# Optimization experiments

Hardware: AMD Instinct MI355X
Metric: run time of the kernel (lower is better)

The kernel has to match this reference:

```python
import jax, jax.numpy as jnp
import numpy as np

L = 32      # num_layer
N_ORD = 64  # order_of_a_LTImodel
U = 64      # u_size
Y = 64      # y_size
T = 8192    # sequence length
SCALE = 0.05  # keep block-bidiagonal A spectrally stable over 8192 steps


def setup_inputs() -> dict:
    key = jax.random.key(0)
    k_u, k_a, k_b0, k_bl, k_c = jax.random.split(key, 5)
    inp = {
        "input": jax.random.normal(k_u, (T, U), dtype=jnp.float32),
        # per-layer A_i weights (diagonal blocks)
        "A_stack": jax.random.normal(k_a, (L, N_ORD, N_ORD), dtype=jnp.float32) * SCALE,
        # layer-0 B (maps u -> state)
        "B0": jax.random.normal(k_b0, (N_ORD, U), dtype=jnp.float32) * SCALE,
        # layer i>=1 B weights (sub-diagonal coupling blocks)
        "B_lower": jax.random.normal(k_bl, (L - 1, N_ORD, N_ORD), dtype=jnp.float32) * SCALE,
        # per-layer C_i weights, concatenated along columns in forward
        "C_stack": jax.random.normal(k_c, (L, Y, N_ORD), dtype=jnp.float32),
        # D is frozen zeros (feedthrough=False)
        "D_w": jnp.zeros((Y, U), dtype=jnp.float32),
    }
    return inp


def _assemble(A_stack, B0, B_lower, C_stack):
    l, n, _ = A_stack.shape
    S = l * n
    A = jnp.zeros((S, S), A_stack.dtype)
    for i in range(l):  # fixed small structural loop
        A = A.at[i * n:(i + 1) * n, i * n:(i + 1) * n].set(A_stack[i])
    for i in range(1, l):
        A = A.at[i * n:(i + 1) * n, (i - 1) * n:i * n].set(B_lower[i - 1])
    B = jnp.concatenate([B0, jnp.zeros((S - n, B0.shape[1]), B0.dtype)], axis=0)
    # torch.cat([C_i], dim=1): [Y, L*n]
    C = jnp.transpose(C_stack, (1, 0, 2)).reshape(C_stack.shape[1], S)
    return A, B, C


def reference(input, A_stack, B0, B_lower, C_stack, D_w):
    A, B, C = _assemble(A_stack, B0, B_lower, C_stack)
    S = A.shape[0]
    x0 = jnp.zeros((S,), input.dtype)

    def step(x, u):
        y = C @ x + D_w @ u      # output BEFORE state update (y_t uses x_t)
        x_next = A @ x + B @ u
        return x_next, y

    _, ys = jax.lax.scan(step, x0, input)
    return ys  # [T, Y]
```

## Files before the change

kernel.cpp:

```cpp
#include <hip/hip_runtime.h>


#define LYR 32
#define NO  64
#define TSEQ 8192
#define PAD 32
#define PR2 (TSEQ+PAD)
#define PB2 ((size_t)PR2*NO)
#define KQ  2048

typedef _Float16 h16;
typedef _Float16 h16x8 __attribute__((ext_vector_type(8)));
typedef float    f32x4 __attribute__((ext_vector_type(4)));

#define MFMA16(a,b,c) __builtin_amdgcn_mfma_f32_16x16x32_f16((a),(b),(c),0,0,0)

__global__ __launch_bounds__(256) void prep_build(
    const float* __restrict__ u, const float* __restrict__ B0,
    const float* __restrict__ Bl, const float* __restrict__ Cst,
    const float* __restrict__ Ast,
    h16* __restrict__ xq, h16* __restrict__ ccast,
    h16* __restrict__ SN, h16* __restrict__ ST,
    h16* __restrict__ ktq, float* __restrict__ Dacc)
{
    __shared__ float sm[3*64*68];
    const int tid = threadIdx.x;

    if (blockIdx.x < 32) {
        const int layer = blockIdx.x;
        float* la = sm;
        float* kc = sm + 64*68;
        float* kn = sm + 2*64*68;
        const float* k0 = (layer == 0) ? B0 : (Bl + (size_t)(layer-1)*4096);
        const float* Aw = Ast + (size_t)layer*4096;
        for (int e = tid; e < 4096; e += 256) {
            int rr = e >> 6, cc = e & 63;
            kc[rr*68 + cc] = k0[e];
            la[rr*68 + cc] = Aw[e];
        }
        __syncthreads();
        const int r0 = (tid >> 4) << 2;
        const int c0 = (tid & 15) << 2;
        for (int j = 0; j < 16; j++) {
            if (j > 0) {
                __syncthreads();
                float acc[4][4] = {};
                for (int k = 0; k < 64; k++) {
                    float a0 = la[(r0+0)*68 + k];
                    float a1 = la[(r0+1)*68 + k];
                    float a2 = la[(r0+2)*68 + k];
                    float a3 = la[(r0+3)*68 + k];
                    f32x4 bv = *(const f32x4*)&kc[k*68 + c0];
                    #pragma unroll
                    for (int jj = 0; jj < 4; jj++) {
                        acc[0][jj] += a0*bv[jj]; acc[1][jj] += a1*bv[jj];
                        acc[2][jj] += a2*bv[jj]; acc[3][jj] += a3*bv[jj];
                    }
                }
                #pragma unroll
                for (int i2 = 0; i2 < 4; i2++) {
                    f32x4 o; o[0]=acc[i2][0]; o[1]=acc[i2][1]; o[2]=acc[i2][2]; o[3]=acc[i2][3];
                    *(f32x4*)&kn[(r0+i2)*68 + c0] = o;
                }
                __syncthreads();
                float* tmp = kc; kc = kn; kn = tmp;
            }
            size_t base = (size_t)(layer*16 + j)*4096;
            for (int e8 = tid; e8 < 512; e8 += 256) {
                int n = e8 >> 3, m0 = (e8 & 7) << 3;
                h16 o[8];
                #pragma unroll
                for (int t = 0; t < 8; t++) o[t] = (h16)kc[n*68 + m0 + t];
                *(int4*)&SN[base + (size_t)n*64 + m0] = *(int4*)&o[0];
                h16 o2[8];
                #pragma unroll
                for (int t = 0; t < 8; t++) o2[t] = (h16)kc[(m0+t)*68 + n];
                *(int4*)&ST[base + (size_t)n*64 + m0] = *(int4*)&o2[0];
            }
        }
        return;
    }

    const int s1 = 256;
    const int s2 = 65536;
    const int s3 = 1792;
    const int s4 = 16384;
    const int s5 = 131072;
    const int s6 = 262144;
    const int total = s1+s2+s3+s4+s5+s6;
    const int4 z4 = make_int4(0,0,0,0);
    for (int e0 = (blockIdx.x - 32)*256 + tid; e0 < total; e0 += 512*256) {
        int e = e0;
        if (e < s1) { *(int4*)&xq[e*8] = z4; continue; }
        e -= s1;
        if (e < s2) {
            int el = e*8;
            f32x4 f0 = *(const f32x4*)&u[el];
            f32x4 f1 = *(const f32x4*)&u[el+4];
            h16 ov[8];
            #pragma unroll
            for (int j = 0; j < 4; j++) { ov[j] = (h16)f0[j]; ov[4+j] = (h16)f1[j]; }
            *(int4*)&xq[PAD*NO + el] = *(int4*)&ov[0];
            continue;
        }
        e -= s2;
        if (e < s3) {
            int b = e >> 8, off = (e & 255)*8;
            *(int4*)&xq[(size_t)(b+1)*PB2 + off] = z4;
            continue;
        }
        e -= s3;
        if (e < s4) {
            int el = e*8;
            f32x4 f0 = *(const f32x4*)&Cst[el];
            f32x4 f1 = *(const f32x4*)&Cst[el+4];
            h16 ov[8];
            #pragma unroll
            for (int j = 0; j < 4; j++) { ov[j] = (h16)f0[j]; ov[4+j] = (h16)f1[j]; }
            *(int4*)&ccast[el] = *(int4*)&ov[0];
            continue;
        }
        e -= s4;
        if (e < s5) { *(int4*)&ktq[e*8] = z4; continue; }
        e -= s5;
        *(int4*)&Dacc[e*4] = z4;
    }
}

__device__ __forceinline__ void comp_mm(const h16* __restrict__ X,
                                        const h16* __restrict__ Y,
                                        int wv, int r, int q, f32x4 acc[4])
{
    h16x8 a0 = *(const h16x8*)(X + (wv*16 + r)*64 + q*8);
    h16x8 a1 = *(const h16x8*)(X + (wv*16 + r)*64 + 32 + q*8);
    #pragma unroll
    for (int c = 0; c < 4; c++) {
        h16x8 b0 = *(const h16x8*)(Y + (c*16 + r)*64 + q*8);
        h16x8 b1 = *(const h16x8*)(Y + (c*16 + r)*64 + 32 + q*8);
        acc[c] = MFMA16(a0, b0, acc[c]);
        acc[c] = MFMA16(a1, b1, acc[c]);
    }
}

__global__ __launch_bounds__(256) void compose2(
    const h16* __restrict__ SN, const h16* __restrict__ ST,
    const h16* __restrict__ cc, h16* __restrict__ P2T,
    float* __restrict__ Dacc)
{
    const int tid = threadIdx.x, wv = tid>>6, lane = tid&63, r = lane&15, q = lane>>4;
    f32x4 acc[4] = {};
    int bid = blockIdx.x;
    if (bid < 248) {
        int g = bid / 31, m2 = bid % 31;
        int j0 = m2 > 15 ? m2 - 15 : 0;
        int j1 = m2 < 15 ? m2 : 15;
        const h16* X = SN + ((size_t)(4*g+1)*16 + j0)*4096;
        const h16* Y = ST + ((size_t)(4*g)*16 + (m2 - j0))*4096;
        for (int it = 0; it <= j1 - j0; ++it) {
            comp_mm(X, Y, wv, r, q, acc);
            X += 4096; Y -= 4096;
        }
        h16* o = P2T + ((size_t)g*31 + m2)*4096;
        #pragma unroll
        for (int c = 0; c < 4; c++)
            #pragma unroll
            for (int g4 = 0; g4 < 4; g4++)
                o[(c*16+r)*64 + wv*16 + q*4 + g4] = (h16)acc[c][g4];
    } else {
        int idx = bid - 248, g = idx >> 4, j = idx & 15;
        comp_mm(cc + (size_t)(4*g)*4096, ST + ((size_t)(4*g)*16 + j)*4096, wv, r, q, acc);
        float* Dd = Dacc + ((size_t)g*32 + j)*4096;
        #pragma unroll
        for (int c = 0; c < 4; c++)
            #pragma unroll
            for (int g4 = 0; g4 < 4; g4++)
                atomicAdd(&Dd[(wv*16 + q*4 + g4)*64 + c*16 + r], acc[c][g4]);
    }
}

__global__ __launch_bounds__(256) void compose3(
    const h16* __restrict__ SN, const h16* __restrict__ cc,
    const h16* __restrict__ P2T, h16* __restrict__ P3T,
    float* __restrict__ Dacc)
{
    const int tid = threadIdx.x, wv = tid>>6, lane = tid&63, r = lane&15, q = lane>>4;
    f32x4 acc[4] = {};
    int bid = blockIdx.x;
    if (bid < 240) {
        int g = bid / 30, m3 = bid % 30;
        int j1 = m3 < 15 ? m3 : 15;
        const h16* X = SN + ((size_t)(4*g+2)*16)*4096;
        const h16* Y = P2T + ((size_t)g*31 + m3)*4096;
        for (int it = 0; it <= j1; ++it) {
            comp_mm(X, Y, wv, r, q, acc);
            X += 4096; Y -= 4096;
        }
        h16* o = P3T + ((size_t)g*30 + m3)*4096;
        #pragma unroll
        for (int c = 0; c < 4; c++)
            #pragma unroll
            for (int g4 = 0; g4 < 4; g4++)
                o[(c*16+r)*64 + wv*16 + q*4 + g4] = (h16)acc[c][g4];
    } else {
        int idx = bid - 240, g = idx / 31, m2 = idx % 31;
        comp_mm(cc + (size_t)(4*g+1)*4096, P2T + ((size_t)g*31 + m2)*4096, wv, r, q, acc);
        float* Dd = Dacc + ((size_t)g*32 + m2 + 1)*4096;
        #pragma unroll
        for (int c = 0; c < 4; c++)
            #pragma unroll
            for (int g4 = 0; g4 < 4; g4++)
                atomicAdd(&Dd[(wv*16 + q*4 + g4)*64 + c*16 + r], acc[c][g4]);
    }
}

__global__ __launch_bounds__(256) void compose4(
    const h16* __restrict__ SN, const h16* __restrict__ cc,
    const h16* __restrict__ P3T, h16* __restrict__ ktq,
    float* __restrict__ Dacc)
{
    __shared__ h16 ldsT[64*72];
    const int tid = threadIdx.x, wv = tid>>6, lane = tid&63, r = lane&15, q = lane>>4;
    f32x4 acc[4] = {};
    int bid = blockIdx.x;
    if (bid < 232) {
        int g = bid / 29, m4 = bid % 29;
        int j1 = m4 < 15 ? m4 : 15;
        const h16* X = SN + ((size_t)(4*g+3)*16)*4096;
        const h16* Y = P3T + ((size_t)g*30 + m4)*4096;
        for (int it = 0; it <= j1; ++it) {
            comp_mm(X, Y, wv, r, q, acc);
            X += 4096; Y -= 4096;
        }
        h16* kq = ktq + (size_t)g*131072 + (size_t)(28 - m4)*64;
        #pragma unroll
        for (int c = 0; c < 4; c++)
            #pragma unroll
            for (int g4 = 0; g4 < 4; g4++) {
                h16 v = (h16)acc[c][g4];
                kq[(size_t)(wv*16 + q*4 + g4)*KQ + c*16 + r] = v;
                ldsT[(c*16+r)*72 + wv*16 + q*4 + g4] = v;
            }
        __syncthreads();
        f32x4 acc2[4] = {};
        const h16* Xc = cc + (size_t)(4*g+3)*4096;
        h16x8 a0 = *(const h16x8*)(Xc + (wv*16 + r)*64 + q*8);
        h16x8 a1 = *(const h16x8*)(Xc + (wv*16 + r)*64 + 32 + q*8);
        #pragma unroll
        for (int c = 0; c < 4; c++) {
            h16x8 b0 = *(const h16x8*)(&ldsT[(c*16+r)*72 + q*8]);
            h16x8 b1 = *(const h16x8*)(&ldsT[(c*16+r)*72 + 32 + q*8]);
            acc2[c] = MFMA16(a0, b0, acc2[c]);
            acc2[c] = MFMA16(a1, b1, acc2[c]);
        }
        float* Dd = Dacc + ((size_t)g*32 + m4 + 3)*4096;
        #pragma unroll
        for (int c = 0; c < 4; c++)
            #pragma unroll
            for (int g4 = 0; g4 < 4; g4++)
                atomicAdd(&Dd[(wv*16 + q*4 + g4)*64 + c*16 + r], acc2[c][g4]);
    } else {
        int idx = bid - 232, g = idx / 30, m3 = idx % 30;
        comp_mm(cc + (size_t)(4*g+2)*4096, P3T + ((size_t)g*30 + m3)*4096, wv, r, q, acc);
        float* Dd = Dacc + ((size_t)g*32 + m3 + 2)*4096;
        #pragma unroll
        for (int c = 0; c < 4; c++)
            #pragma unroll
            for (int g4 = 0; g4 < 4; g4++)
                atomicAdd(&Dd[(wv*16 + q*4 + g4)*64 + c*16 + r], acc[c][g4]);
    }
}

__global__ __launch_bounds__(256) void castD(const float* __restrict__ Dacc,
                                             h16* __restrict__ ktd)
{
    const int total4 = 8*32*4096/4;
    for (int idx4 = blockIdx.x*256 + threadIdx.x; idx4 < total4; idx4 += 256*256) {
        int idx = idx4 << 2;
        int gdo = idx >> 12;
        int g = gdo >> 5, dd = gdo & 31;
        int rem = idx & 4095;
        int y = rem >> 6, m = rem & 63;
        f32x4 f = *(const f32x4*)&Dacc[idx];
        h16 o4[4];
        #pragma unroll
        for (int t = 0; t < 4; t++) o4[t] = (h16)f[t];
        *(int2*)&ktd[(size_t)g*131072 + (size_t)y*KQ + (31 - dd)*64 + m] = *(int2*)&o4[0];
    }
}

template<int WRST>
__global__ __launch_bounds__(512) void stage(
    const h16* __restrict__ pin, h16* __restrict__ pout,
    const h16* __restrict__ ktqg, const h16* __restrict__ ktdg,
    float* __restrict__ out, int first)
{
    __shared__ __align__(16) h16   win[64*72];
    __shared__ __align__(16) float red[4*32*68];
    const int tid = threadIdx.x;
    const size_t t0 = (size_t)blockIdx.x * 32;

    {
        int rr = tid >> 3, cc = tid & 7;
        *(int4*)&win[rr*72 + cc*8] = *(const int4*)&pin[(t0 + rr)*64 + cc*8];
    }
    __syncthreads();

    const int wv = tid >> 6, lane = tid & 63, r = lane & 15, q = lane >> 4;
    const int half = wv >> 2, kq = wv & 3;
    const bool active = WRST || (half == 1);
    f32x4 acc[2][4] = {};
    if (active) {
        const h16* kb = half ? ktdg : ktqg;
        const h16* abase = &win[(r + kq*8)*72 + q*8];
        const h16* bbase = kb + (size_t)r*KQ + kq*512 + q*8;
#define LDA(s, ls) (*(const h16x8*)(abase + ((s)*16 + ((ls)>>1))*72 + ((ls)&1)*32))
#define LDB(c, ls) (*(const h16x8*)(bbase + (size_t)(c)*(16*KQ) + (ls)*32))
        h16x8 a[2][2], b[2][4];
        #pragma unroll
        for (int sl = 0; sl < 2; sl++) {
            #pragma unroll
            for (int s = 0; s < 2; s++) a[sl][s] = LDA(s, sl);
            #pragma unroll
            for (int c = 0; c < 4; c++) b[sl][c] = LDB(c, sl);
        }
        #pragma unroll
        for (int ls = 0; ls < 16; ls++) {
            h16x8 ca[2], cb[4];
            #pragma unroll
            for (int s = 0; s < 2; s++) ca[s] = a[ls&1][s];
            #pragma unroll
            for (int c = 0; c < 4; c++) cb[c] = b[ls&1][c];
            if (ls < 14) {
                #pragma unroll
                for (int s = 0; s < 2; s++) a[ls&1][s] = LDA(s, ls+2);
                #pragma unroll
                for (int c = 0; c < 4; c++) b[ls&1][c] = LDB(c, ls+2);
            }
            #pragma unroll
            for (int s = 0; s < 2; s++)
                #pragma unroll
                for (int c = 0; c < 4; c++)
                    acc[s][c] = MFMA16(ca[s], cb[c], acc[s][c]);
        }
#undef LDA
#undef LDB
    }

    const int rh = half * (2*32*68);
    __syncthreads();
    if (active && kq >= 2) {
        float* myred = red + rh + (kq-2)*(32*68);
        #pragma unroll
        for (int s2 = 0; s2 < 2; s2++)
            #pragma unroll
            for (int c = 0; c < 4; c++)
                #pragma unroll
                for (int g4 = 0; g4 < 4; g4++)
                    myred[(s2*16 + q*4 + g4)*68 + c*16 + r] = acc[s2][c][g4];
    }
    __syncthreads();
    if (active && kq < 2) {
        float* myred = red + rh + kq*(32*68);
        #pragma unroll
        for (int s2 = 0; s2 < 2; s2++)
            #pragma unroll
            for (int c = 0; c < 4; c++)
                #pragma unroll
                for (int g4 = 0; g4 < 4; g4++)
                    myred[(s2*16 + q*4 + g4)*68 + c*16 + r] += acc[s2][c][g4];
    }
    __syncthreads();
    if (WRST && tid < 256) {
        int orow = tid >> 3, cb2 = (tid & 7) << 3;
        f32x4 u0 = *(const f32x4*)&red[orow*68 + cb2];
        f32x4 u1 = *(const f32x4*)&red[orow*68 + cb2 + 4];
        f32x4 v0 = *(const f32x4*)&red[32*68 + orow*68 + cb2];
        f32x4 v1 = *(const f32x4*)&red[32*68 + orow*68 + cb2 + 4];
        u0 += v0; u1 += v1;
        h16 ov[8];
        #pragma unroll
        for (int j = 0; j < 4; j++) { ov[j] = (h16)u0[j]; ov[4+j] = (h16)u1[j]; }
        *(int4*)&pout[(PAD + t0 + orow)*64 + cb2] = *(int4*)&ov[0];
    }
    if (tid >= 256) {
        int t2 = tid - 256;
        int orow = t2 >> 3, cb2 = (t2 & 7) << 3;
        const float* base = red + 2*32*68;
        f32x4 u0 = *(const f32x4*)&base[orow*68 + cb2];
        f32x4 u1 = *(const f32x4*)&base[orow*68 + cb2 + 4];
        f32x4 v0 = *(const f32x4*)&base[32*68 + orow*68 + cb2];
        f32x4 v1 = *(const f32x4*)&base[32*68 + orow*68 + cb2 + 4];
        u0 += v0; u1 += v1;
        float* op = out + (t0 + orow)*64 + cb2;
        if (first) {
            *(f32x4*)op = u0; *(f32x4*)(op+4) = u1;
        } else {
            f32x4 o0 = *(f32x4*)op, o1 = *(f32x4*)(op+4);
            o0 += u0; o1 += u1;
            *(f32x4*)op = o0; *(f32x4*)(op+4) = o1;
        }
    }
}

extern "C" void kernel_launch(void* const* d_in, const int* in_sizes, int n_in,
                              void* d_out, int out_size, void* d_ws, size_t ws_size,
                              hipStream_t stream)
{
    const float* u   = (const float*)d_in[0];
    const float* Ast = (const float*)d_in[1];
    const float* B0  = (const float*)d_in[2];
    const float* Bl  = (const float*)d_in[3];
    const float* Cst = (const float*)d_in[4];
    float* out = (float*)d_out;
    (void)in_sizes; (void)n_in; (void)out_size; (void)ws_size;

    char* ws = (char*)d_ws;
    h16*   xq    = (h16*)ws;
    h16*   ccast = (h16*)(ws + 8421376);
    h16*   SN    = (h16*)(ws + 8683520);
    h16*   ST    = (h16*)(ws + 12877824);
    h16*   P2T   = (h16*)(ws + 17072128);
    h16*   P3T   = (h16*)(ws + 19103744);
    h16*   ktq   = (h16*)(ws + 21069824);
    h16*   ktd   = (h16*)(ws + 23166976);
    float* Dacc  = (float*)(ws + 25264128);

    prep_build<<<544, 256, 0, stream>>>(u, B0, Bl, Cst, Ast, xq, ccast, SN, ST, ktq, Dacc);
    compose2<<<376, 256, 0, stream>>>(SN, ST, ccast, P2T, Dacc);
    compose3<<<488, 256, 0, stream>>>(SN, ccast, P2T, P3T, Dacc);
    compose4<<<472, 256, 0, stream>>>(SN, ccast, P3T, ktq, Dacc);
    castD<<<256, 256, 0, stream>>>(Dacc, ktd);
    for (int g = 0; g < 7; g++) {
        stage<1><<<256, 512, 0, stream>>>(xq + (size_t)g*PB2, xq + (size_t)(g+1)*PB2,
                                          ktq + (size_t)g*131072, ktd + (size_t)g*131072,
                                          out, g == 0);
    }
    stage<0><<<256, 512, 0, stream>>>(xq + (size_t)7*PB2, xq,
                                      ktq + (size_t)7*131072, ktd + (size_t)7*131072,
                                      out, 0);
}
```

Measured before the change: 319.7 us.

## Use MFMA for layer power build, skip unused SN/ST writes, widen stage tile

The per-layer power computation in prep_build switches from scalar FP32 FMA loops to f16 MFMA with a transposed half-precision copy kept in shared memory. It also writes SN or ST depending on the layer index instead of always writing both. The stage kernel now handles 64 timesteps per block instead of 32, so each loaded kernel-weight fragment is reused across twice as many rows, and it launches half as many blocks. In exchange the stage kernel uses more registers and has fewer blocks to spread across CUs, and the recurrence products are now accumulated from f16-rounded operands instead of full FP32.

```diff
diff --git a/kernel.cpp b/kernel.cpp
--- a/kernel.cpp
+++ b/kernel.cpp
@@ -23,60 +23,73 @@
     h16* __restrict__ SN, h16* __restrict__ ST,
     h16* __restrict__ ktq, float* __restrict__ Dacc)
 {
-    __shared__ float sm[3*64*68];
+    __shared__ __align__(16) h16   Ah[64*72];
+    __shared__ __align__(16) h16   kT[64*72];
+    __shared__ __align__(16) float kf[64*68];
     const int tid = threadIdx.x;
 
     if (blockIdx.x < 32) {
         const int layer = blockIdx.x;
-        float* la = sm;
-        float* kc = sm + 64*68;
-        float* kn = sm + 2*64*68;
+        const bool wantST = (layer & 3) == 0;
         const float* k0 = (layer == 0) ? B0 : (Bl + (size_t)(layer-1)*4096);
         const float* Aw = Ast + (size_t)layer*4096;
-        for (int e = tid; e < 4096; e += 256) {
-            int rr = e >> 6, cc = e & 63;
-            kc[rr*68 + cc] = k0[e];
-            la[rr*68 + cc] = Aw[e];
+        for (int e8 = tid; e8 < 512; e8 += 256) {
+            int n = e8 >> 3, m0 = (e8 & 7) << 3;
+            f32x4 a0 = *(const f32x4*)&Aw[n*64 + m0];
+            f32x4 a1 = *(const f32x4*)&Aw[n*64 + m0 + 4];
+            h16 ah[8];
+            #pragma unroll
+            for (int t = 0; t < 4; t++) { ah[t] = (h16)a0[t]; ah[4+t] = (h16)a1[t]; }
+            *(int4*)&Ah[n*72 + m0] = *(int4*)&ah[0];
+            f32x4 b0 = *(const f32x4*)&k0[n*64 + m0];
+            f32x4 b1 = *(const f32x4*)&k0[n*64 + m0 + 4];
+            *(f32x4*)&kf[n*68 + m0]     = b0;
+            *(f32x4*)&kf[n*68 + m0 + 4] = b1;
         }
         __syncthreads();
-        const int r0 = (tid >> 4) << 2;
-        const int c0 = (tid & 15) << 2;
+
+        const int wv = tid >> 6, lane = tid & 63, r = lane & 15, q = lane >> 4;
+        const h16x8 a0 = *(const h16x8*)&Ah[(wv*16 + r)*72 + q*8];
+        const h16x8 a1 = *(const h16x8*)&Ah[(wv*16 + r)*72 + 32 + q*8];
+
         for (int j = 0; j < 16; j++) {
             if (j > 0) {
+                f32x4 acc[4] = {};
+                #pragma unroll
+                for (int c = 0; c < 4; c++) {
+                    h16x8 b0 = *(const h16x8*)&kT[(c*16 + r)*72 + q*8];
+                    h16x8 b1 = *(const h16x8*)&kT[(c*16 + r)*72 + 32 + q*8];
+                    acc[c] = MFMA16(a0, b0, acc[c]);
+                    acc[c] = MFMA16(a1, b1, acc[c]);
+                }
+                #pragma unroll
+                for (int c = 0; c < 4; c++)
+                    #pragma unroll
+                    for (int g4 = 0; g4 < 4; g4++)
+                        kf[(wv*16 + q*4 + g4)*68 + c*16 + r] = acc[c][g4];
                 __syncthreads();
-                float acc[4][4] = {};
-                for (int k = 0; k < 64; k++) {
-                    float a0 = la[(r0+0)*68 + k];
-                    float a1 = la[(r0+1)*68 + k];
-                    float a2 = la[(r0+2)*68 + k];
-                    float a3 = la[(r0+3)*68 + k];
-                    f32x4 bv = *(const f32x4*)&kc[k*68 + c0];
-                    #pragma unroll
-                    for (int jj = 0; jj < 4; jj++) {
-                        acc[0][jj] += a0*bv[jj]; acc[1][jj] += a1*bv[jj];
-                        acc[2][jj] += a2*bv[jj]; acc[3][jj] += a3*bv[jj];
-                    }
-                }
-                #pragma unroll
-                for (int i2 = 0; i2 < 4; i2++) {
-                    f32x4 o; o[0]=acc[i2][0]; o[1]=acc[i2][1]; o[2]=acc[i2][2]; o[3]=acc[i2][3];
-                    *(f32x4*)&kn[(r0+i2)*68 + c0] = o;
-                }
-                __syncthreads();
-                float* tmp = kc; kc = kn; kn = tmp;
             }
             size_t base = (size_t)(layer*16 + j)*4096;
             for (int e8 = tid; e8 < 512; e8 += 256) {
                 int n = e8 >> 3, m0 = (e8 & 7) << 3;
+                f32x4 v0 = *(const f32x4*)&kf[n*68 + m0];
+                f32x4 v1 = *(const f32x4*)&kf[n*68 + m0 + 4];
                 h16 o[8];
                 #pragma unroll
-                for (int t = 0; t < 8; t++) o[t] = (h16)kc[n*68 + m0 + t];
-                *(int4*)&SN[base + (size_t)n*64 + m0] = *(int4*)&o[0];
-                h16 o2[8];
-                #pragma unroll
-                for (int t = 0; t < 8; t++) o2[t] = (h16)kc[(m0+t)*68 + n];
-                *(int4*)&ST[base + (size_t)n*64 + m0] = *(int4*)&o2[0];
+                for (int t = 0; t < 4; t++) { o[t] = (h16)v0[t]; o[4+t] = (h16)v1[t]; }
+                if (!wantST)
+                    *(int4*)&SN[base + (size_t)n*64 + m0] = *(int4*)&o[0];
+                #pragma unroll
+                for (int t = 0; t < 8; t++)
+                    kT[(m0 + t)*72 + n] = o[t];
+                if (wantST) {
+                    h16 o2[8];
+                    #pragma unroll
+                    for (int t = 0; t < 8; t++) o2[t] = (h16)kf[(m0 + t)*68 + n];
+                    *(int4*)&ST[base + (size_t)n*64 + m0] = *(int4*)&o2[0];
+                }
             }
+            __syncthreads();
         }
         return;
     }
@@ -294,13 +307,13 @@
     const h16* __restrict__ ktqg, const h16* __restrict__ ktdg,
     float* __restrict__ out, int first)
 {
-    __shared__ __align__(16) h16   win[64*72];
+    __shared__ __align__(16) h16   win[96*72];
     __shared__ __align__(16) float red[4*32*68];
     const int tid = threadIdx.x;
-    const size_t t0 = (size_t)blockIdx.x * 32;
-
-    {
-        int rr = tid >> 3, cc = tid & 7;
+    const size_t t0 = (size_t)blockIdx.x * 64;
+
+    for (int e = tid; e < 96*8; e += 512) {
+        int rr = e >> 3, cc = e & 7;
         *(int4*)&win[rr*72 + cc*8] = *(const int4*)&pin[(t0 + rr)*64 + cc*8];
     }
     __syncthreads();
@@ -308,96 +321,107 @@
     const int wv = tid >> 6, lane = tid & 63, r = lane & 15, q = lane >> 4;
     const int half = wv >> 2, kq = wv & 3;
     const bool active = WRST || (half == 1);
-    f32x4 acc[2][4] = {};
+    f32x4 acc[2][2][4] = {};
     if (active) {
         const h16* kb = half ? ktdg : ktqg;
         const h16* abase = &win[(r + kq*8)*72 + q*8];
         const h16* bbase = kb + (size_t)r*KQ + kq*512 + q*8;
-#define LDA(s, ls) (*(const h16x8*)(abase + ((s)*16 + ((ls)>>1))*72 + ((ls)&1)*32))
+#define LDA(st, s, ls) (*(const h16x8*)(abase + ((st)*32 + (s)*16 + ((ls)>>1))*72 + ((ls)&1)*32))
 #define LDB(c, ls) (*(const h16x8*)(bbase + (size_t)(c)*(16*KQ) + (ls)*32))
-        h16x8 a[2][2], b[2][4];
+        h16x8 a[2][2][2], b[2][4];
         #pragma unroll
         for (int sl = 0; sl < 2; sl++) {
             #pragma unroll
-            for (int s = 0; s < 2; s++) a[sl][s] = LDA(s, sl);
+            for (int st = 0; st < 2; st++)
+                #pragma unroll
+                for (int s = 0; s < 2; s++) a[sl][st][s] = LDA(st, s, sl);
             #pragma unroll
             for (int c = 0; c < 4; c++) b[sl][c] = LDB(c, sl);
         }
         #pragma unroll
         for (int ls = 0; ls < 16; ls++) {
-            h16x8 ca[2], cb[4];
-            #pragma unroll
-            for (int s = 0; s < 2; s++) ca[s] = a[ls&1][s];
+            h16x8 ca[2][2], cb[4];
+            #pragma unroll
+            for (int st = 0; st < 2; st++)
+                #pragma unroll
+                for (int s = 0; s < 2; s++) ca[st][s] = a[ls&1][st][s];
             #pragma unroll
             for (int c = 0; c < 4; c++) cb[c] = b[ls&1][c];
             if (ls < 14) {
                 #pragma unroll
-                for (int s = 0; s < 2; s++) a[ls&1][s] = LDA(s, ls+2);
+                for (int st = 0; st < 2; st++)
+                    #pragma unroll
+                    for (int s = 0; s < 2; s++) a[ls&1][st][s] = LDA(st, s, ls+2);
                 #pragma unroll
                 for (int c = 0; c < 4; c++) b[ls&1][c] = LDB(c, ls+2);
             }
             #pragma unroll
-            for (int s = 0; s < 2; s++)
-                #pragma unroll
-                for (int c = 0; c < 4; c++)
-                    acc[s][c] = MFMA16(ca[s], cb[c], acc[s][c]);
+            for (int st = 0; st < 2; st++)
+                #pragma unroll
+                for (int s = 0; s < 2; s++)
+                    #pragma unroll
+                    for (int c = 0; c < 4; c++)
+                        acc[st][s][c] = MFMA16(ca[st][s], cb[c], acc[st][s][c]);
         }
 #undef LDA
 #undef LDB
     }
 
     const int rh = half * (2*32*68);
-    __syncthreads();
-    if (active && kq >= 2) {
-        float* myred = red + rh + (kq-2)*(32*68);
-        #pragma unroll
-        for (int s2 = 0; s2 < 2; s2++)
-            #pragma unroll
-            for (int c = 0; c < 4; c++)
-                #pragma unroll
-                for (int g4 = 0; g4 < 4; g4++)
-                    myred[(s2*16 + q*4 + g4)*68 + c*16 + r] = acc[s2][c][g4];
-    }
-    __syncthreads();
-    if (active && kq < 2) {
-        float* myred = red + rh + kq*(32*68);
-        #pragma unroll
-        for (int s2 = 0; s2 < 2; s2++)
-            #pragma unroll
-            for (int c = 0; c < 4; c++)
-                #pragma unroll
-                for (int g4 = 0; g4 < 4; g4++)
-                    myred[(s2*16 + q*4 + g4)*68 + c*16 + r] += acc[s2][c][g4];
-    }
-    __syncthreads();
-    if (WRST && tid < 256) {
-        int orow = tid >> 3, cb2 = (tid & 7) << 3;
-        f32x4 u0 = *(const f32x4*)&red[orow*68 + cb2];
-        f32x4 u1 = *(const f32x4*)&red[orow*68 + cb2 + 4];
-        f32x4 v0 = *(const f32x4*)&red[32*68 + orow*68 + cb2];
-        f32x4 v1 = *(const f32x4*)&red[32*68 + orow*68 + cb2 + 4];
-        u0 += v0; u1 += v1;
-        h16 ov[8];
-        #pragma unroll
-        for (int j = 0; j < 4; j++) { ov[j] = (h16)u0[j]; ov[4+j] = (h16)u1[j]; }
-        *(int4*)&pout[(PAD + t0 + orow)*64 + cb2] = *(int4*)&ov[0];
-    }
-    if (tid >= 256) {
-        int t2 = tid - 256;
-        int orow = t2 >> 3, cb2 = (t2 & 7) << 3;
-        const float* base = red + 2*32*68;
-        f32x4 u0 = *(const f32x4*)&base[orow*68 + cb2];
-        f32x4 u1 = *(const f32x4*)&base[orow*68 + cb2 + 4];
-        f32x4 v0 = *(const f32x4*)&base[32*68 + orow*68 + cb2];
-        f32x4 v1 = *(const f32x4*)&base[32*68 + orow*68 + cb2 + 4];
-        u0 += v0; u1 += v1;
-        float* op = out + (t0 + orow)*64 + cb2;
-        if (first) {
-            *(f32x4*)op = u0; *(f32x4*)(op+4) = u1;
-        } else {
-            f32x4 o0 = *(f32x4*)op, o1 = *(f32x4*)(op+4);
-            o0 += u0; o1 += u1;
-            *(f32x4*)op = o0; *(f32x4*)(op+4) = o1;
+    #pragma unroll
+    for (int st = 0; st < 2; st++) {
+        __syncthreads();
+        if (active && kq >= 2) {
+            float* myred = red + rh + (kq-2)*(32*68);
+            #pragma unroll
+            for (int s2 = 0; s2 < 2; s2++)
+                #pragma unroll
+                for (int c = 0; c < 4; c++)
+                    #pragma unroll
+                    for (int g4 = 0; g4 < 4; g4++)
+                        myred[(s2*16 + q*4 + g4)*68 + c*16 + r] = acc[st][s2][c][g4];
+        }
+        __syncthreads();
+        if (active && kq < 2) {
+            float* myred = red + rh + kq*(32*68);
+            #pragma unroll
+            for (int s2 = 0; s2 < 2; s2++)
+                #pragma unroll
+                for (int c = 0; c < 4; c++)
+                    #pragma unroll
+                    for (int g4 = 0; g4 < 4; g4++)
+                        myred[(s2*16 + q*4 + g4)*68 + c*16 + r] += acc[st][s2][c][g4];
+        }
+        __syncthreads();
+        if (WRST && tid < 256) {
+            int orow = tid >> 3, cb2 = (tid & 7) << 3;
+            f32x4 u0 = *(const f32x4*)&red[orow*68 + cb2];
+            f32x4 u1 = *(const f32x4*)&red[orow*68 + cb2 + 4];
+            f32x4 v0 = *(const f32x4*)&red[32*68 + orow*68 + cb2];
+            f32x4 v1 = *(const f32x4*)&red[32*68 + orow*68 + cb2 + 4];
+            u0 += v0; u1 += v1;
+            h16 ov[8];
+            #pragma unroll
+            for (int j = 0; j < 4; j++) { ov[j] = (h16)u0[j]; ov[4+j] = (h16)u1[j]; }
+            *(int4*)&pout[(PAD + t0 + st*32 + orow)*64 + cb2] = *(int4*)&ov[0];
+        }
+        if (tid >= 256) {
+            int t2 = tid - 256;
+            int orow = t2 >> 3, cb2 = (t2 & 7) << 3;
+            const float* base = red + 2*32*68;
+            f32x4 u0 = *(const f32x4*)&base[orow*68 + cb2];
+            f32x4 u1 = *(const f32x4*)&base[orow*68 + cb2 + 4];
+            f32x4 v0 = *(const f32x4*)&base[32*68 + orow*68 + cb2];
+            f32x4 v1 = *(const f32x4*)&base[32*68 + orow*68 + cb2 + 4];
+            u0 += v0; u1 += v1;
+            float* op = out + (t0 + st*32 + orow)*64 + cb2;
+            if (first) {
+                *(f32x4*)op = u0; *(f32x4*)(op+4) = u1;
+            } else {
+                f32x4 o0 = *(f32x4*)op, o1 = *(f32x4*)(op+4);
+                o0 += u0; o1 += u1;
+                *(f32x4*)op = o0; *(f32x4*)(op+4) = o1;
+            }
         }
     }
 }
@@ -431,11 +455,11 @@
     compose4<<<472, 256, 0, stream>>>(SN, ccast, P3T, ktq, Dacc);
     castD<<<256, 256, 0, stream>>>(Dacc, ktd);
     for (int g = 0; g < 7; g++) {
-        stage<1><<<256, 512, 0, stream>>>(xq + (size_t)g*PB2, xq + (size_t)(g+1)*PB2,
-                                          ktq + (size_t)g*131072, ktd + (size_t)g*131072,
-                                          out, g == 0);
-    }
-    stage<0><<<256, 512, 0, stream>>>(xq + (size_t)7*PB2, xq,
-                                      ktq + (size_t)7*131072, ktd + (size_t)7*131072,
-                                      out, 0);
-}
+        stage<1><<<TSEQ/64, 512, 0, stream>>>(xq + (size_t)g*PB2, xq + (size_t)(g+1)*PB2,
+                                              ktq + (size_t)g*131072, ktd + (size_t)g*131072,
+                                              out, g == 0);
+    }
+    stage<0><<<TSEQ/64, 512, 0, stream>>>(xq + (size_t)7*PB2, xq,
+                                          ktq + (size_t)7*131072, ktd + (size_t)7*131072,
+                                          out, 0);
+}
```

Result: faster. 303.0 us (-5.2%).
